# Optimization experiments

Measured on AMD Instinct MI355X. Metric: run time of the kernel, lower is better.

Reference implementation:

```python
import jax, jax.numpy as jnp
import numpy as np

N, E = 50000, 800000
F_IN, H, C = 128, 8, 32  # hidden=256, heads=8 -> C=32
DROP_P = 0.6


def setup_inputs() -> dict:
    key = jax.random.key(0)
    ks = jax.random.split(key, 8)
    x = jax.random.normal(ks[0], (N, F_IN), dtype=jnp.float32)
    edge_index = jax.random.randint(ks[1], (2, E), 0, N, dtype=jnp.int64)
    # precomputed inverted-dropout masks (Bernoulli keep * 1/(1-p)), as passed via dp_mask args
    dp_mask = (jax.random.uniform(ks[2], (E, H)) > DROP_P).astype(jnp.float32) / (1.0 - DROP_P)
    dp_mask_self = (jax.random.uniform(ks[3], (N, H)) > DROP_P).astype(jnp.float32) / (1.0 - DROP_P)
    # learned parameters of GATConv
    W = jax.random.normal(ks[4], (F_IN, H * C), dtype=jnp.float32) * (1.0 / np.sqrt(F_IN))
    att_src = jax.random.normal(ks[5], (H, C), dtype=jnp.float32) * 0.1
    att_dst = jax.random.normal(ks[6], (H, C), dtype=jnp.float32) * 0.1
    bias = jnp.zeros((H * C,), dtype=jnp.float32)
    return {"x": x, "edge_index": edge_index, "dp_mask": dp_mask,
            "dp_mask_self": dp_mask_self, "W": W, "att_src": att_src,
            "att_dst": att_dst, "bias": bias}


def reference(x, edge_index, dp_mask, dp_mask_self, W, att_src, att_dst, bias):
    n = x.shape[0]
    h = (x @ W).reshape(n, H, C)                      # [N,H,C]
    a_src = jnp.sum(h * att_src, axis=-1)             # [N,H] source-side score
    a_dst = jnp.sum(h * att_dst, axis=-1)             # [N,H] dest-side score
    # flow='target_to_source': aggregate at edge_index[0], gather from edge_index[1]
    dst = edge_index[0]
    src = edge_index[1]
    e_alpha = jax.nn.leaky_relu(a_src[src] + a_dst[dst], 0.2)   # [E,H]
    s_alpha = jax.nn.leaky_relu(a_src + a_dst, 0.2)             # [N,H] self-loops
    seg = jnp.concatenate([dst, jnp.arange(n, dtype=dst.dtype)])
    alpha = jnp.concatenate([e_alpha, s_alpha], axis=0)         # [E+N,H]
    # segment softmax over each destination's neighborhood (incl. self-loop)
    m = jax.ops.segment_max(alpha, seg, num_segments=n)
    ex = jnp.exp(alpha - m[seg])
    denom = jax.ops.segment_sum(ex, seg, num_segments=n)
    p = ex / denom[seg]                                         # [E+N,H]
    # dropout on attention coefficients (masks passed in)
    p = p * jnp.concatenate([dp_mask, dp_mask_self], axis=0)
    msgs = jnp.concatenate([h[src], h], axis=0)                 # [E+N,H,C]
    out = jax.ops.segment_sum(p[:, :, None] * msgs, seg, num_segments=n)
    return out.reshape(n, H * C) + bias                         # concat heads + bias
```

## Files before the change

### kernel.cpp

```cpp
#include <hip/hip_runtime.h>

#define NN 50000
#define FIN 128
#define HC 256
#define NH 8
#define NE 800000
#define WROW 136
#define GEMMB 391
#define NBLK1 3516
#define OVFCAP 131072

typedef __attribute__((ext_vector_type(8))) short short8;
typedef __attribute__((ext_vector_type(4))) short short4v;
typedef __attribute__((ext_vector_type(4))) float floatx4;

__device__ __forceinline__ float bf2f(unsigned short u) {
    union { unsigned int i; float f; } v; v.i = ((unsigned int)u) << 16; return v.f;
}
__device__ __forceinline__ unsigned short f2bf(float f) {
    union { float f; unsigned int i; } v; v.f = f;
    unsigned int r = v.i + 0x7fffu + ((v.i >> 16) & 1u);
    return (unsigned short)(r >> 16);
}
__device__ __forceinline__ float lrelu(float x) { return x > 0.f ? x : 0.2f * x; }
__device__ __forceinline__ float ldf(const void* p, int f32, long long i) {
    return f32 ? ((const float*)p)[i] : bf2f(((const unsigned short*)p)[i]);
}
__device__ __forceinline__ int lde(const int* ei, int i64, long long i) {
    return i64 ? (int)((const long long*)ei)[i] : ei[i];
}
__device__ __forceinline__ float sel8(const float s[2][4], int t2, int rr) {
    float a0 = t2 ? s[1][0] : s[0][0];
    float a1 = t2 ? s[1][1] : s[0][1];
    float a2 = t2 ? s[1][2] : s[0][2];
    float a3 = t2 ? s[1][3] : s[0][3];
    return (rr == 0) ? a0 : ((rr == 1) ? a1 : ((rr == 2) ? a2 : a3));
}

__global__ __launch_bounds__(256) void k_front(
        const void* __restrict__ x, const int* __restrict__ ei,
        const void* __restrict__ dpm, const void* __restrict__ W,
        const void* __restrict__ as_, const void* __restrict__ ad_,
        int* __restrict__ flags, unsigned short* __restrict__ h,
        float* __restrict__ a_src, float* __restrict__ a_dst,
        int* __restrict__ cnt, int* __restrict__ ovfcnt,
        unsigned int* __restrict__ bucket, int2* __restrict__ ovf, int cap) {
    __shared__ unsigned short lwt[256 * WROW];
    __shared__ int s_bad, s_nz;
    const int tid = threadIdx.x;
    const int b = blockIdx.x;

    if (tid == 0) { s_bad = 0; s_nz = 0; }
    __syncthreads();
    {
        unsigned int wv = ((const unsigned int*)dpm)[tid];
        if (wv != 0u && wv != 0x40200000u) atomicAdd(&s_bad, 1);
        if (((const unsigned int*)ei)[2 * tid + 1] != 0u) atomicAdd(&s_nz, 1);
    }
    __syncthreads();
    const int f32 = (s_bad == 0) ? 1 : 0;
    const int i64 = (s_nz == 0) ? 1 : 0;
    if (b == 0 && tid == 0) { flags[0] = f32; flags[1] = i64; }

    if (b < GEMMB) {
        {
            if (f32) {
                const float* wp = (const float*)W + tid;
                for (int k = 0; k < FIN; k++) lwt[tid * WROW + k] = f2bf(wp[(long long)k * HC]);
            } else {
                const unsigned short* wp = (const unsigned short*)W + tid;
                for (int k = 0; k < FIN; k++) lwt[tid * WROW + k] = wp[(long long)k * HC];
            }
        }
        __syncthreads();

        const int lane = tid & 63;
        const int wave = tid >> 6;
        const int lrow = lane & 15;
        const int quad = lane >> 4;
        const int row0w = b * 128 + wave * 32;

        short8 a[2][4];
        #pragma unroll
        for (int t = 0; t < 2; t++)
            #pragma unroll
            for (int q = 0; q < 4; q++)
                #pragma unroll
                for (int j = 0; j < 8; j++) a[t][q][j] = 0;

        #pragma unroll
        for (int t = 0; t < 2; t++) {
            int row = row0w + t * 16 + lrow;
            if (row < NN) {
                if (f32) {
                    const float* xp = (const float*)x + (long long)row * FIN + quad * 8;
                    #pragma unroll
                    for (int q = 0; q < 4; q++) {
                        floatx4 u0 = *(const floatx4*)(xp + q * 32);
                        floatx4 u1 = *(const floatx4*)(xp + q * 32 + 4);
                        #pragma unroll
                        for (int j = 0; j < 4; j++) {
                            a[t][q][j]     = (short)f2bf(u0[j]);
                            a[t][q][j + 4] = (short)f2bf(u1[j]);
                        }
                    }
                } else {
                    const unsigned short* xp = (const unsigned short*)x + (long long)row * FIN + quad * 8;
                    #pragma unroll
                    for (int q = 0; q < 4; q++) a[t][q] = *(const short8*)(xp + q * 32);
                }
            }
        }

        float sS[2][4], sD[2][4];
        #pragma unroll 4
        for (int ct = 0; ct < 16; ct++) {
            if ((ct & 1) == 0) {
                #pragma unroll
                for (int t = 0; t < 2; t++)
                    #pragma unroll
                    for (int r = 0; r < 4; r++) { sS[t][r] = 0.f; sD[t][r] = 0.f; }
            }
            floatx4 acc0 = {0.f, 0.f, 0.f, 0.f};
            floatx4 acc1 = {0.f, 0.f, 0.f, 0.f};
            const unsigned short* wp = lwt + (ct * 16 + lrow) * WROW + quad * 8;
            #pragma unroll
            for (int q = 0; q < 4; q++) {
                short8 bb = *(const short8*)(wp + q * 32);
                acc0 = __builtin_amdgcn_mfma_f32_16x16x32_bf16(a[0][q], bb, acc0, 0, 0, 0);
                acc1 = __builtin_amdgcn_mfma_f32_16x16x32_bf16(a[1][q], bb, acc1, 0, 0, 0);
            }
            #pragma unroll
            for (int r = 0; r < 4; r++) {
                int orow = row0w + quad * 4 + r;
                if (orow < NN) h[(long long)orow * HC + ct * 16 + lrow] = f2bf(acc0[r]);
                int orow1 = orow + 16;
                if (orow1 < NN) h[(long long)orow1 * HC + ct * 16 + lrow] = f2bf(acc1[r]);
            }
            float tS = ldf(as_, f32, ct * 16 + lrow);
            float tD = ldf(ad_, f32, ct * 16 + lrow);
            #pragma unroll
            for (int r = 0; r < 4; r++) {
                sS[0][r] += acc0[r] * tS;  sS[1][r] += acc1[r] * tS;
                sD[0][r] += acc0[r] * tD;  sD[1][r] += acc1[r] * tD;
            }
            if (ct & 1) {
                #pragma unroll
                for (int m = 1; m <= 8; m <<= 1)
                    #pragma unroll
                    for (int t = 0; t < 2; t++)
                        #pragma unroll
                        for (int r = 0; r < 4; r++) {
                            sS[t][r] += __shfl_xor(sS[t][r], m);
                            sD[t][r] += __shfl_xor(sD[t][r], m);
                        }
                int hd = ct >> 1;
                if (lrow < 8) {
                    int t2 = lrow >> 2, rr = lrow & 3;
                    int row = row0w + t2 * 16 + quad * 4 + rr;
                    if (row < NN) a_src[row * NH + hd] = sel8(sS, t2, rr);
                } else {
                    int lr = lrow - 8;
                    int t2 = lr >> 2, rr = lr & 3;
                    int row = row0w + t2 * 16 + quad * 4 + rr;
                    if (row < NN) a_dst[row * NH + hd] = sel8(sD, t2, rr);
                }
            }
        }
    } else {
        int e = (b - GEMMB) * 256 + tid;
        int dst = lde(ei, i64, e);
        int src = lde(ei, i64, (long long)NE + e);
        unsigned int msk = 0;
        if (f32) {
            const floatx4* dp = (const floatx4*)((const float*)dpm + (long long)e * 8);
            floatx4 d0 = dp[0], d1 = dp[1];
            #pragma unroll
            for (int j = 0; j < 4; j++) {
                msk |= (d0[j] != 0.f ? 1u : 0u) << j;
                msk |= (d1[j] != 0.f ? 1u : 0u) << (4 + j);
            }
        } else {
            short8 dd = *(const short8*)((const unsigned short*)dpm + (long long)e * 8);
            #pragma unroll
            for (int j = 0; j < 8; j++) msk |= (dd[j] != 0 ? 1u : 0u) << j;
        }
        unsigned int entry = (unsigned int)src | (msk << 16);
        int pos = atomicAdd(&cnt[dst], 1);
        if (pos < cap) bucket[(long long)dst * cap + pos] = entry;
        else {
            int op = atomicAdd(ovfcnt, 1);
            if (op < OVFCAP) ovf[op] = make_int2(dst, (int)entry);
        }
    }
}

__global__ __launch_bounds__(256) void k_aggr(
        const int* __restrict__ cnt, const int* __restrict__ ovfcnt,
        const unsigned int* __restrict__ bucket, const int2* __restrict__ ovf,
        const float* __restrict__ a_src, const float* __restrict__ a_dst,
        const unsigned short* __restrict__ h, const void* __restrict__ dps,
        const int* __restrict__ flags, const void* __restrict__ bs_,
        void* __restrict__ out, int cap) {
    int node = blockIdx.x * 4 + (threadIdx.x >> 6);
    int lane = threadIdx.x & 63;
    if (node >= NN) return;
    const int f32 = flags[0];
    int novf = *ovfcnt; novf = novf > OVFCAP ? OVFCAP : novf;
    int c = cnt[node];
    int mn = c < cap ? c : cap;
    long long base = (long long)node * cap;

    const int hh = lane >> 3;
    const int cb = lane * 4;
    float adst = a_dst[node * NH + hh];
    float dn = 0.f;
    float acc0 = 0.f, acc1 = 0.f, acc2 = 0.f, acc3 = 0.f;

    unsigned int ubuf = (lane < mn) ? bucket[base + lane] : 0u;
    for (int b0 = 0; b0 < mn; b0 += 64) {
        int nidx = b0 + 64 + lane;
        unsigned int unext = (nidx < mn) ? bucket[base + nidx] : 0u;
        int lim = min(64, mn - b0);
        int j = 0;
        for (; j + 8 <= lim; j += 8) {
            unsigned int u[8]; float g[8]; short4v hv[8];
            #pragma unroll
            for (int k = 0; k < 8; k++) u[k] = __shfl(ubuf, j + k);
            #pragma unroll
            for (int k = 0; k < 8; k++) g[k] = a_src[(int)(u[k] & 0xFFFFu) * NH + hh];
            #pragma unroll
            for (int k = 0; k < 8; k++) {
                hv[k][0] = 0; hv[k][1] = 0; hv[k][2] = 0; hv[k][3] = 0;
                if ((u[k] >> (16 + hh)) & 1u)
                    hv[k] = *(const short4v*)(h + (long long)(u[k] & 0xFFFFu) * HC + cb);
            }
            #pragma unroll
            for (int k = 0; k < 8; k++) {
                float w = __expf(lrelu(g[k] + adst));
                dn += w;
                float p = w * 2.5f;
                acc0 += p * bf2f((unsigned short)hv[k][0]);
                acc1 += p * bf2f((unsigned short)hv[k][1]);
                acc2 += p * bf2f((unsigned short)hv[k][2]);
                acc3 += p * bf2f((unsigned short)hv[k][3]);
            }
        }
        for (; j < lim; j++) {
            unsigned int u = __shfl(ubuf, j);
            int src = (int)(u & 0xFFFFu);
            float w = __expf(lrelu(a_src[src * NH + hh] + adst));
            dn += w;
            if ((u >> (16 + hh)) & 1u) {
                short4v hv = *(const short4v*)(h + (long long)src * HC + cb);
                float p = w * 2.5f;
                acc0 += p * bf2f((unsigned short)hv[0]);
                acc1 += p * bf2f((unsigned short)hv[1]);
                acc2 += p * bf2f((unsigned short)hv[2]);
                acc3 += p * bf2f((unsigned short)hv[3]);
            }
        }
        ubuf = unext;
    }
    for (int i = 0; i < novf; i++) {
        int2 tv = ovf[i];
        if (tv.x == node) {
            unsigned int u = (unsigned int)tv.y;
            int src = (int)(u & 0xFFFFu);
            float w = __expf(lrelu(a_src[src * NH + hh] + adst));
            dn += w;
            if ((u >> (16 + hh)) & 1u) {
                short4v hv = *(const short4v*)(h + (long long)src * HC + cb);
                float p = w * 2.5f;
                acc0 += p * bf2f((unsigned short)hv[0]);
                acc1 += p * bf2f((unsigned short)hv[1]);
                acc2 += p * bf2f((unsigned short)hv[2]);
                acc3 += p * bf2f((unsigned short)hv[3]);
            }
        }
    }
    {
        float wS = __expf(lrelu(a_src[node * NH + hh] + adst));
        dn += wS;
        float pS = wS * ldf(dps, f32, (long long)node * NH + hh);
        short4v hv = *(const short4v*)(h + (long long)node * HC + cb);
        acc0 += pS * bf2f((unsigned short)hv[0]);
        acc1 += pS * bf2f((unsigned short)hv[1]);
        acc2 += pS * bf2f((unsigned short)hv[2]);
        acc3 += pS * bf2f((unsigned short)hv[3]);
    }
    float inv = 1.0f / dn;
    float b0 = ldf(bs_, f32, cb + 0), b1 = ldf(bs_, f32, cb + 1);
    float b2 = ldf(bs_, f32, cb + 2), b3 = ldf(bs_, f32, cb + 3);
    if (f32) {
        floatx4 o = {acc0 * inv + b0, acc1 * inv + b1, acc2 * inv + b2, acc3 * inv + b3};
        *(floatx4*)((float*)out + (long long)node * HC + cb) = o;
    } else {
        short4v o;
        o[0] = (short)f2bf(acc0 * inv + b0);
        o[1] = (short)f2bf(acc1 * inv + b1);
        o[2] = (short)f2bf(acc2 * inv + b2);
        o[3] = (short)f2bf(acc3 * inv + b3);
        *(short4v*)((unsigned short*)out + (long long)node * HC + cb) = o;
    }
}

extern "C" void kernel_launch(void* const* d_in, const int* in_sizes, int n_in,
                              void* d_out, int out_size, void* d_ws, size_t ws_size,
                              hipStream_t stream) {
    const void* x       = d_in[0];
    const int*  ei      = (const int*)d_in[1];
    const void* dp_mask = d_in[2];
    const void* dp_self = d_in[3];
    const void* W       = d_in[4];
    const void* att_s   = d_in[5];
    const void* att_d   = d_in[6];
    const void* bias    = d_in[7];

    char* w = (char*)d_ws;
    unsigned short* h      = (unsigned short*)(w + 0);
    float*          a_src  = (float*)(w + 25600000);
    float*          a_dst  = (float*)(w + 27200000);
    int*            cnt    = (int*)(w + 28800000);
    int*            ovfcnt = (int*)(w + 29000000);
    int*            flags  = (int*)(w + 29000064);
    int2*           ovf    = (int2*)(w + 29000960);
    unsigned int*   bucket = (unsigned int*)(w + 30049536);

    long long avail = (long long)ws_size - 30049536LL;
    int cap = (int)(avail / 200000LL);
    if (cap > 64) cap = 64;
    if (cap < 4) cap = 4;

    hipMemsetAsync(cnt, 0, 200960, stream);
    k_front<<<NBLK1, 256, 0, stream>>>(x, ei, dp_mask, W, att_s, att_d,
                                       flags, h, a_src, a_dst, cnt, ovfcnt, bucket, ovf, cap);
    k_aggr<<<NN / 4, 256, 0, stream>>>(cnt, ovfcnt, bucket, ovf, a_src, a_dst, h,
                                       dp_self, flags, bias, d_out, cap);
}
```

Before: 230.6 us.

## Restructure edge aggregation: per-lane edge weights shared via bpermute, scalar bucket loads

The aggregation loop now loads bucket entries with wave-uniform scalar loads and computes each edge's attention weight once per (edge, head), on 8 lanes per head, instead of having every lane recompute it. Weights are broadcast with ds_bpermute and the dropout bit is carried in the sign. The denominator is combined with an xor-shuffle reduction, and bf16 unpacking uses shift/mask on uint2 loads with fma. This removes redundant exp and a_src gathers plus the vector shuffles, at the cost of reading bucket entries past the per-node count, which is why the workspace tail is reserved.

```diff
diff --git a/kernel.cpp b/kernel.cpp
--- a/kernel.cpp
+++ b/kernel.cpp
@@ -35,6 +35,15 @@
     float a2 = t2 ? s[1][2] : s[0][2];
     float a3 = t2 ? s[1][3] : s[0][3];
     return (rr == 0) ? a0 : ((rr == 1) ? a1 : ((rr == 2) ? a2 : a3));
+}
+__device__ __forceinline__ float blo(unsigned int u) {
+    union { unsigned int i; float f; } v; v.i = u << 16; return v.f;
+}
+__device__ __forceinline__ float bhi(unsigned int u) {
+    union { unsigned int i; float f; } v; v.i = u & 0xFFFF0000u; return v.f;
+}
+__device__ __forceinline__ float bperm(int addr, float v) {
+    return __uint_as_float((unsigned int)__builtin_amdgcn_ds_bpermute(addr, (int)__float_as_uint(v)));
 }
 
 __global__ __launch_bounds__(256) void k_front(
@@ -205,63 +214,59 @@
     int node = blockIdx.x * 4 + (threadIdx.x >> 6);
     int lane = threadIdx.x & 63;
     if (node >= NN) return;
+    const int unode = __builtin_amdgcn_readfirstlane(node);
     const int f32 = flags[0];
     int novf = *ovfcnt; novf = novf > OVFCAP ? OVFCAP : novf;
-    int c = cnt[node];
-    int mn = c < cap ? c : cap;
-    long long base = (long long)node * cap;
+    int mn = cnt[unode]; mn = mn < cap ? mn : cap;
+    const unsigned int* __restrict__ bp = bucket + (long long)unode * cap;
 
     const int hh = lane >> 3;
+    const int e8 = lane & 7;
+    const int badr = (lane & 56) << 2;
     const int cb = lane * 4;
-    float adst = a_dst[node * NH + hh];
-    float dn = 0.f;
+    const float adst = a_dst[unode * NH + hh];
+
+    float dnp = 0.f;
     float acc0 = 0.f, acc1 = 0.f, acc2 = 0.f, acc3 = 0.f;
 
-    unsigned int ubuf = (lane < mn) ? bucket[base + lane] : 0u;
-    for (int b0 = 0; b0 < mn; b0 += 64) {
-        int nidx = b0 + 64 + lane;
-        unsigned int unext = (nidx < mn) ? bucket[base + nidx] : 0u;
-        int lim = min(64, mn - b0);
-        int j = 0;
-        for (; j + 8 <= lim; j += 8) {
-            unsigned int u[8]; float g[8]; short4v hv[8];
-            #pragma unroll
-            for (int k = 0; k < 8; k++) u[k] = __shfl(ubuf, j + k);
-            #pragma unroll
-            for (int k = 0; k < 8; k++) g[k] = a_src[(int)(u[k] & 0xFFFFu) * NH + hh];
-            #pragma unroll
-            for (int k = 0; k < 8; k++) {
-                hv[k][0] = 0; hv[k][1] = 0; hv[k][2] = 0; hv[k][3] = 0;
-                if ((u[k] >> (16 + hh)) & 1u)
-                    hv[k] = *(const short4v*)(h + (long long)(u[k] & 0xFFFFu) * HC + cb);
-            }
-            #pragma unroll
-            for (int k = 0; k < 8; k++) {
-                float w = __expf(lrelu(g[k] + adst));
-                dn += w;
-                float p = w * 2.5f;
-                acc0 += p * bf2f((unsigned short)hv[k][0]);
-                acc1 += p * bf2f((unsigned short)hv[k][1]);
-                acc2 += p * bf2f((unsigned short)hv[k][2]);
-                acc3 += p * bf2f((unsigned short)hv[k][3]);
-            }
-        }
-        for (; j < lim; j++) {
-            unsigned int u = __shfl(ubuf, j);
-            int src = (int)(u & 0xFFFFu);
-            float w = __expf(lrelu(a_src[src * NH + hh] + adst));
-            dn += w;
-            if ((u >> (16 + hh)) & 1u) {
-                short4v hv = *(const short4v*)(h + (long long)src * HC + cb);
-                float p = w * 2.5f;
-                acc0 += p * bf2f((unsigned short)hv[0]);
-                acc1 += p * bf2f((unsigned short)hv[1]);
-                acc2 += p * bf2f((unsigned short)hv[2]);
-                acc3 += p * bf2f((unsigned short)hv[3]);
-            }
-        }
-        ubuf = unext;
-    }
+    for (int j = 0; j < mn; j += 8) {
+        unsigned int u0 = bp[j + 0], u1 = bp[j + 1], u2 = bp[j + 2], u3 = bp[j + 3],
+                     u4 = bp[j + 4], u5 = bp[j + 5], u6 = bp[j + 6], u7 = bp[j + 7];
+
+        int idx = j + e8;
+        int idxc = idx < mn ? idx : mn - 1;
+        unsigned int ue = bp[idxc];
+        int esrc = (int)(ue & 0xFFFFu);
+        float al = a_src[esrc * NH + hh] + adst;
+        float w = __expf(fmaxf(al, 0.2f * al));
+        w = idx < mn ? w : 0.f;
+        dnp += w;
+        float ws = ((ue >> (16 + hh)) & 1u) ? w : -w;
+
+        #define GATW(K) float w##K = bperm(badr + 4 * K, ws);
+        GATW(0) GATW(1) GATW(2) GATW(3) GATW(4) GATW(5) GATW(6) GATW(7)
+        #undef GATW
+
+        #define GATH(K) \
+            const unsigned short* hp##K = h + \
+                (((long long)(__builtin_amdgcn_readfirstlane((int)u##K) & 0xFFFF)) << 8); \
+            uint2 v##K = make_uint2(0u, 0u); \
+            if (w##K > 0.f) v##K = *(const uint2*)(hp##K + cb);
+        GATH(0) GATH(1) GATH(2) GATH(3) GATH(4) GATH(5) GATH(6) GATH(7)
+        #undef GATH
+
+        #define MACC(K) { float p = w##K * 2.5f; \
+            acc0 = fmaf(p, blo(v##K.x), acc0); acc1 = fmaf(p, bhi(v##K.x), acc1); \
+            acc2 = fmaf(p, blo(v##K.y), acc2); acc3 = fmaf(p, bhi(v##K.y), acc3); }
+        MACC(0) MACC(1) MACC(2) MACC(3) MACC(4) MACC(5) MACC(6) MACC(7)
+        #undef MACC
+    }
+
+    dnp += __shfl_xor(dnp, 1);
+    dnp += __shfl_xor(dnp, 2);
+    dnp += __shfl_xor(dnp, 4);
+    float dn = dnp;
+
     for (int i = 0; i < novf; i++) {
         int2 tv = ovf[i];
         if (tv.x == node) {
@@ -270,24 +275,20 @@
             float w = __expf(lrelu(a_src[src * NH + hh] + adst));
             dn += w;
             if ((u >> (16 + hh)) & 1u) {
-                short4v hv = *(const short4v*)(h + (long long)src * HC + cb);
+                uint2 hv = *(const uint2*)(h + ((long long)src << 8) + cb);
                 float p = w * 2.5f;
-                acc0 += p * bf2f((unsigned short)hv[0]);
-                acc1 += p * bf2f((unsigned short)hv[1]);
-                acc2 += p * bf2f((unsigned short)hv[2]);
-                acc3 += p * bf2f((unsigned short)hv[3]);
+                acc0 = fmaf(p, blo(hv.x), acc0); acc1 = fmaf(p, bhi(hv.x), acc1);
+                acc2 = fmaf(p, blo(hv.y), acc2); acc3 = fmaf(p, bhi(hv.y), acc3);
             }
         }
     }
     {
-        float wS = __expf(lrelu(a_src[node * NH + hh] + adst));
+        float wS = __expf(lrelu(a_src[unode * NH + hh] + adst));
         dn += wS;
-        float pS = wS * ldf(dps, f32, (long long)node * NH + hh);
-        short4v hv = *(const short4v*)(h + (long long)node * HC + cb);
-        acc0 += pS * bf2f((unsigned short)hv[0]);
-        acc1 += pS * bf2f((unsigned short)hv[1]);
-        acc2 += pS * bf2f((unsigned short)hv[2]);
-        acc3 += pS * bf2f((unsigned short)hv[3]);
+        float pS = wS * ldf(dps, f32, (long long)unode * NH + hh);
+        uint2 hv = *(const uint2*)(h + ((long long)unode << 8) + cb);
+        acc0 = fmaf(pS, blo(hv.x), acc0); acc1 = fmaf(pS, bhi(hv.x), acc1);
+        acc2 = fmaf(pS, blo(hv.y), acc2); acc3 = fmaf(pS, bhi(hv.y), acc3);
     }
     float inv = 1.0f / dn;
     float b0 = ldf(bs_, f32, cb + 0), b1 = ldf(bs_, f32, cb + 1);
@@ -327,7 +328,7 @@
     int2*           ovf    = (int2*)(w + 29000960);
     unsigned int*   bucket = (unsigned int*)(w + 30049536);
 
-    long long avail = (long long)ws_size - 30049536LL;
+    long long avail = (long long)ws_size - 30049536LL - 256LL;
     int cap = (int)(avail / 200000LL);
     if (cap > 64) cap = 64;
     if (cap < 4) cap = 4;
```

Result: faster. 215.8 us (-6.4%).
